# Optimization experiments

Hardware: AMD Instinct MI355X
Metric: run time of the kernel (lower is better)

Reference implementation:

```python
import jax, jax.numpy as jnp
import numpy as np

N = 50000          # nodes
E = 800000         # edges (before self-loops)
IN_DIM = 128
HIDDEN = 128
HEADS = 8
C = HIDDEN // HEADS  # 16, per-head dim
NEG_SLOPE = 0.2


def setup_inputs() -> dict:
    key = jax.random.key(0)
    ks = jax.random.split(key, 12)
    s = 0.1
    return {
        "x": jax.random.normal(ks[0], (N, IN_DIM), jnp.float32),
        "W1": jax.random.normal(ks[1], (IN_DIM, HIDDEN), jnp.float32) * s,
        "b1": jnp.zeros((HIDDEN,), jnp.float32),
        "att_l1": jax.random.normal(ks[2], (1, HEADS, C), jnp.float32) * s,
        "att_r1": jax.random.normal(ks[3], (1, HEADS, C), jnp.float32) * s,
        "W2": jax.random.normal(ks[4], (HIDDEN, HIDDEN), jnp.float32) * s,
        "b2": jnp.zeros((HIDDEN,), jnp.float32),
        "att_l2": jax.random.normal(ks[5], (1, HEADS, C), jnp.float32) * s,
        "att_r2": jax.random.normal(ks[6], (1, HEADS, C), jnp.float32) * s,
        "fcW": jax.random.normal(ks[7], (HIDDEN, 1), jnp.float32) * s,
        "fcb": jnp.zeros((1,), jnp.float32),
        "edge_index": jax.random.randint(ks[8], (2, E), 0, N, jnp.int32),
    }


def supergat_layer(h, W, b, att_l, att_r, src, dst):
    """SuperGATConv (attention_type='MX', concat=True), eval mode (no dropout).
    src/dst already include self-loops. h: [N, F_in]."""
    xt = (h @ W).reshape(N, HEADS, C)            # [N, H, C]
    x_j = xt[src]                                # source (message) feats [Etot, H, C]
    x_i = xt[dst]                                # target feats           [Etot, H, C]
    # MX attention: alpha = (a_l . x_j + a_r . x_i) * sigmoid(x_i . x_j)
    logits = jnp.sum(x_i * x_j, axis=-1)         # [Etot, H]
    alpha = jnp.sum(x_j * att_l, axis=-1) + jnp.sum(x_i * att_r, axis=-1)
    alpha = alpha * jax.nn.sigmoid(logits)
    alpha = jax.nn.leaky_relu(alpha, NEG_SLOPE)
    # segment softmax over incoming edges of each target node
    amax = jax.lax.stop_gradient(jax.ops.segment_max(alpha, dst, num_segments=N))
    ex = jnp.exp(alpha - amax[dst])
    denom = jax.ops.segment_sum(ex, dst, num_segments=N)
    attn = ex / (denom[dst] + 1e-16)             # [Etot, H]
    out = jax.ops.segment_sum(x_j * attn[..., None], dst, num_segments=N)  # [N, H, C]
    return out.reshape(N, HEADS * C) + b


def reference(x, W1, b1, att_l1, att_r1, W2, b2, att_l2, att_r2, fcW, fcb, edge_index):
    # add self-loops once (SuperGATConv add_self_loops=True)
    loops = jnp.arange(N, dtype=edge_index.dtype)
    src = jnp.concatenate([edge_index[0], loops])
    dst = jnp.concatenate([edge_index[1], loops])
    gelu = lambda t: jax.nn.gelu(t, approximate=False)
    h = gelu(supergat_layer(x, W1, b1, att_l1, att_r1, src, dst))   # dropout = identity (eval)
    h = gelu(supergat_layer(h, W2, b2, att_l2, att_r2, src, dst))
    return h @ fcW + fcb                          # [N, 1]
```

## Files before the change

### kernel.cpp

```cpp
#include <hip/hip_runtime.h>
#include <hip/hip_fp16.h>
#include <math.h>

#define N_NODES 50000
#define N_EDGES 800000
#define ETOT (N_EDGES + N_NODES)
#define F 128
#define SCAN_B 256
#define NSCAN ((N_NODES + SCAN_B - 1) / SCAN_B)
#define BM 128
#define LOG2E 1.44269504088896341f

typedef _Float16 h2 __attribute__((ext_vector_type(2)));

__device__ __forceinline__ float dpp_xor1(float v) {
    int b = __builtin_amdgcn_update_dpp(0, __float_as_int(v), 0xB1, 0xF, 0xF, true);
    return v + __int_as_float(b);
}


__global__ void k_count(const int* __restrict__ ei, int* __restrict__ counts) {
    int base = (blockIdx.x * 256 + threadIdx.x) * 8;
    if (base < N_EDGES) {
        int4 a = *(const int4*)(ei + N_EDGES + base);
        int4 b = *(const int4*)(ei + N_EDGES + base + 4);
        atomicAdd(&counts[a.x], 1); atomicAdd(&counts[a.y], 1);
        atomicAdd(&counts[a.z], 1); atomicAdd(&counts[a.w], 1);
        atomicAdd(&counts[b.x], 1); atomicAdd(&counts[b.y], 1);
        atomicAdd(&counts[b.z], 1); atomicAdd(&counts[b.w], 1);
    }
}

__global__ void k_scan1(const int* __restrict__ counts, int* __restrict__ indptr,
                        int* __restrict__ bsums) {
    __shared__ int s[SCAN_B];
    int i = blockIdx.x * SCAN_B + threadIdx.x;
    int v = (i < N_NODES) ? (counts[i] + 1) : 0;
    s[threadIdx.x] = v;
    __syncthreads();
    #pragma unroll
    for (int off = 1; off < SCAN_B; off <<= 1) {
        int t = (threadIdx.x >= off) ? s[threadIdx.x - off] : 0;
        __syncthreads();
        s[threadIdx.x] += t;
        __syncthreads();
    }
    if (i < N_NODES) indptr[i] = s[threadIdx.x] - v;
    if (threadIdx.x == SCAN_B - 1) bsums[blockIdx.x] = s[SCAN_B - 1];
}

__global__ void k_scan2(int* __restrict__ bsums) {
    __shared__ int s[SCAN_B];
    int v = (threadIdx.x < NSCAN) ? bsums[threadIdx.x] : 0;
    s[threadIdx.x] = v;
    __syncthreads();
    #pragma unroll
    for (int off = 1; off < SCAN_B; off <<= 1) {
        int t = (threadIdx.x >= off) ? s[threadIdx.x - off] : 0;
        __syncthreads();
        s[threadIdx.x] += t;
        __syncthreads();
    }
    if (threadIdx.x < NSCAN) bsums[threadIdx.x] = s[threadIdx.x] - v;
}

__global__ void k_scan3_fill(int* __restrict__ indptr, const int* __restrict__ bsums,
                             int* __restrict__ fill, int* __restrict__ srcs) {
    int i = blockIdx.x * SCAN_B + threadIdx.x;
    if (i < N_NODES) {
        int p = indptr[i] + bsums[blockIdx.x];
        indptr[i] = p;
        fill[i] = p + 1;
        srcs[p] = i;
    }
    if (i == 0) indptr[N_NODES] = ETOT;
}

__global__ void k_fill_edges(const int* __restrict__ ei, int* __restrict__ fill,
                             int* __restrict__ srcs) {
    int base = (blockIdx.x * 256 + threadIdx.x) * 8;
    if (base < N_EDGES) {
        int4 sa = *(const int4*)(ei + base);
        int4 sb = *(const int4*)(ei + base + 4);
        int4 da = *(const int4*)(ei + N_EDGES + base);
        int4 db = *(const int4*)(ei + N_EDGES + base + 4);
        int p0 = atomicAdd(&fill[da.x], 1);
        int p1 = atomicAdd(&fill[da.y], 1);
        int p2 = atomicAdd(&fill[da.z], 1);
        int p3 = atomicAdd(&fill[da.w], 1);
        int p4 = atomicAdd(&fill[db.x], 1);
        int p5 = atomicAdd(&fill[db.y], 1);
        int p6 = atomicAdd(&fill[db.z], 1);
        int p7 = atomicAdd(&fill[db.w], 1);
        srcs[p0] = sa.x; srcs[p1] = sa.y; srcs[p2] = sa.z; srcs[p3] = sa.w;
        srcs[p4] = sb.x; srcs[p5] = sb.y; srcs[p6] = sb.z; srcs[p7] = sb.w;
    }
}


__global__ __launch_bounds__(256) void k_gemm(const float* __restrict__ A,
                                              const float* __restrict__ W,
                                              unsigned char* __restrict__ Ch) {
    __shared__ float Ws[F][64];
    int t = threadIdx.x;
    int tile = blockIdx.x >> 1;
    int chf = blockIdx.x & 1;
    int r0 = tile * BM;

    const float4* W4 = (const float4*)W;
    #pragma unroll
    for (int jj = 0; jj < 8; ++jj) {
        int i = t + jj * 256;
        int k = i >> 4;
        int c4 = i & 15;
        *(float4*)&Ws[k][c4 * 4] = W4[k * 32 + chf * 16 + c4];
    }
    __syncthreads();

    int cg = t & 15;
    int rg = t >> 4;
    int rbase = r0 + rg * 8;

    const float4* Ap[8];
    #pragma unroll
    for (int i = 0; i < 8; ++i) {
        int gr = rbase + i;
        if (gr >= N_NODES) gr = N_NODES - 1;
        Ap[i] = (const float4*)A + (size_t)gr * 32;
    }

    float acc[8][4];
    #pragma unroll
    for (int i = 0; i < 8; ++i)
        #pragma unroll
        for (int j = 0; j < 4; ++j) acc[i][j] = 0.f;

    #pragma unroll 2
    for (int kk = 0; kk < 32; ++kk) {
        float4 xr[8];
        #pragma unroll
        for (int i = 0; i < 8; ++i) xr[i] = Ap[i][kk];
        #pragma unroll
        for (int kj = 0; kj < 4; ++kj) {
            int k = kk * 4 + kj;
            float4 wa = *(const float4*)&Ws[k][cg * 4];
            #pragma unroll
            for (int i = 0; i < 8; ++i) {
                float xv = (kj == 0) ? xr[i].x : (kj == 1) ? xr[i].y
                         : (kj == 2) ? xr[i].z : xr[i].w;
                acc[i][0] += xv * wa.x; acc[i][1] += xv * wa.y;
                acc[i][2] += xv * wa.z; acc[i][3] += xv * wa.w;
            }
        }
    }

    int colb = chf * 64 + cg * 4;
    #pragma unroll
    for (int i = 0; i < 8; ++i) {
        int row = rbase + i;
        if (row < N_NODES) {
            _Float16 hh[4];
            hh[0] = (_Float16)acc[i][0]; hh[1] = (_Float16)acc[i][1];
            hh[2] = (_Float16)acc[i][2]; hh[3] = (_Float16)acc[i][3];
            *(uint2*)(Ch + (size_t)row * 256 + colb * 2) = *(const uint2*)hh;
        }
    }
}


__global__ __launch_bounds__(256) void k_attn(
    const unsigned char* __restrict__ xt16,
    const int* __restrict__ indptr, const int* __restrict__ srcs,
    const float* __restrict__ att_l, const float* __restrict__ att_r,
    const float* __restrict__ bias, float* __restrict__ out,
    const float* __restrict__ fcW, const float* __restrict__ fcb, int mode) {

    int wid = threadIdx.x >> 6;
    int lane = threadIdx.x & 63;
    int node = blockIdx.x * 4 + wid;
    if (node >= N_NODES) return;
    int sub = lane >> 4;
    int sl  = lane & 15;

    uint4 xa = *(const uint4*)(xt16 + (size_t)node * 256 + sl * 16);
    h2 xi_h2[4];
    xi_h2[0] = __builtin_bit_cast(h2, xa.x); xi_h2[1] = __builtin_bit_cast(h2, xa.y);
    xi_h2[2] = __builtin_bit_cast(h2, xa.z); xi_h2[3] = __builtin_bit_cast(h2, xa.w);

    const float4* arp = (const float4*)(att_r + sl * 8);
    const float4* alp = (const float4*)(att_l + sl * 8);
    float4 r0 = arp[0], r1 = arp[1];
    float4 l0 = alp[0], l1 = alp[1];
    float rs = (float)xi_h2[0].x*r0.x + (float)xi_h2[0].y*r0.y
             + (float)xi_h2[1].x*r0.z + (float)xi_h2[1].y*r0.w
             + (float)xi_h2[2].x*r1.x + (float)xi_h2[2].y*r1.y
             + (float)xi_h2[3].x*r1.z + (float)xi_h2[3].y*r1.w;
    float ri = LOG2E * dpp_xor1(rs);
    h2 al_h2[4];
    al_h2[0] = h2{(_Float16)(l0.x*LOG2E), (_Float16)(l0.y*LOG2E)};
    al_h2[1] = h2{(_Float16)(l0.z*LOG2E), (_Float16)(l0.w*LOG2E)};
    al_h2[2] = h2{(_Float16)(l1.x*LOG2E), (_Float16)(l1.y*LOG2E)};
    al_h2[3] = h2{(_Float16)(l1.z*LOG2E), (_Float16)(l1.w*LOG2E)};

    float d = 0.f;
    float o[8];
    #pragma unroll
    for (int k = 0; k < 8; ++k) o[k] = 0.f;

    int beg = indptr[node], end = indptr[node + 1];
    int nstep = (end - beg + 3) >> 2;

    int idx = beg + sub;
    bool v0 = idx < end;
    int j0 = srcs[v0 ? idx : beg];
    uint4 ra0 = *(const uint4*)(xt16 + (size_t)j0 * 256 + sl * 16);
    int idx1 = idx + 4;
    bool v1 = idx1 < end;
    int j1 = srcs[v1 ? idx1 : beg];

    for (int s = 0; s < nstep; ++s) {
        uint4 ra1 = *(const uint4*)(xt16 + (size_t)j1 * 256 + sl * 16);
        int idx2 = idx1 + 4;
        bool v2 = idx2 < end;
        int j2 = srcs[v2 ? idx2 : beg];

        h2 xj[4];
        xj[0] = __builtin_bit_cast(h2, ra0.x); xj[1] = __builtin_bit_cast(h2, ra0.y);
        xj[2] = __builtin_bit_cast(h2, ra0.z); xj[3] = __builtin_bit_cast(h2, ra0.w);

        float lg = 0.f, lj = 0.f;
        #pragma unroll
        for (int k = 0; k < 4; ++k) {
            lg = __builtin_amdgcn_fdot2(xi_h2[k], xj[k], lg, false);
            lj = __builtin_amdgcn_fdot2(al_h2[k], xj[k], lj, false);
        }
        lg = dpp_xor1(lg);
        lj = dpp_xor1(lj);

        float sg = __builtin_amdgcn_rcpf(1.f + __builtin_amdgcn_exp2f(-lg * LOG2E));
        float a = (lj + ri) * sg;
        a = fmaxf(a, 0.f) + 0.2f * fminf(a, 0.f);
        a = v0 ? a : -1e30f;
        float e = __builtin_amdgcn_exp2f(a);
        d += e;
        #pragma unroll
        for (int k = 0; k < 4; ++k) {
            o[2*k]   += e * (float)xj[k].x;
            o[2*k+1] += e * (float)xj[k].y;
        }

        ra0 = ra1; v0 = v1; v1 = v2; j1 = j2; idx1 = idx2;
    }

    d += __shfl_xor(d, 16);
    d += __shfl_xor(d, 32);
    #pragma unroll
    for (int k = 0; k < 8; ++k) {
        o[k] += __shfl_xor(o[k], 16);
        o[k] += __shfl_xor(o[k], 32);
    }

    float inv = __builtin_amdgcn_rcpf(d + 1e-16f);
    const float4* bbp = (const float4*)(bias + sl * 8);
    float4 b0 = bbp[0], b1 = bbp[1];
    float bb[8] = {b0.x, b0.y, b0.z, b0.w, b1.x, b1.y, b1.z, b1.w};
    float g[8];
    #pragma unroll
    for (int k = 0; k < 8; ++k) {
        float v = o[k] * inv + bb[k];
        g[k] = 0.5f * v * (1.f + erff(v * 0.70710678118654752f));
    }

    if (mode == 0) {
        if (sub == 0) {
            float4* Co = (float4*)(out + (size_t)node * F + sl * 8);
            Co[0] = make_float4(g[0], g[1], g[2], g[3]);
            Co[1] = make_float4(g[4], g[5], g[6], g[7]);
        }
    } else {
        const float4* fwp = (const float4*)(fcW + sl * 8);
        float4 f0 = fwp[0], f1 = fwp[1];
        float p = g[0]*f0.x + g[1]*f0.y + g[2]*f0.z + g[3]*f0.w
                + g[4]*f1.x + g[5]*f1.y + g[6]*f1.z + g[7]*f1.w;
        p += __shfl_xor(p, 1);
        p += __shfl_xor(p, 2);
        p += __shfl_xor(p, 4);
        p += __shfl_xor(p, 8);
        if (lane == 0) out[node] = p + fcb[0];
    }
}


extern "C" void kernel_launch(void* const* d_in, const int* in_sizes, int n_in,
                              void* d_out, int out_size, void* d_ws, size_t ws_size,
                              hipStream_t stream) {
    const float* x     = (const float*)d_in[0];
    const float* W1    = (const float*)d_in[1];
    const float* b1    = (const float*)d_in[2];
    const float* attl1 = (const float*)d_in[3];
    const float* attr1 = (const float*)d_in[4];
    const float* W2    = (const float*)d_in[5];
    const float* b2    = (const float*)d_in[6];
    const float* attl2 = (const float*)d_in[7];
    const float* attr2 = (const float*)d_in[8];
    const float* fcW   = (const float*)d_in[9];
    const float* fcb   = (const float*)d_in[10];
    const int*   ei    = (const int*)d_in[11];
    float* outp = (float*)d_out;

    float* h1  = (float*)d_ws;
    unsigned char* xt16 = (unsigned char*)(h1 + (size_t)N_NODES * F);
    int* indptr = (int*)(xt16 + (size_t)N_NODES * 256);
    int* fill   = indptr + (N_NODES + 1);
    int* srcs   = fill + N_NODES;
    int* bsums  = srcs + ETOT;
    int* counts = fill;

    int nb_e8 = (N_EDGES / 8 + 255) / 256;

    hipMemsetAsync(counts, 0, N_NODES * sizeof(int), stream);
    k_count<<<nb_e8, 256, 0, stream>>>(ei, counts);
    k_scan1<<<NSCAN, SCAN_B, 0, stream>>>(counts, indptr, bsums);
    k_scan2<<<1, SCAN_B, 0, stream>>>(bsums);
    k_scan3_fill<<<NSCAN, SCAN_B, 0, stream>>>(indptr, bsums, fill, srcs);
    k_fill_edges<<<nb_e8, 256, 0, stream>>>(ei, fill, srcs);

    int nb_g = ((N_NODES + BM - 1) / BM) * 2;
    int nb_a = (N_NODES + 3) / 4;

    k_gemm<<<nb_g, 256, 0, stream>>>(x, W1, xt16);
    k_attn<<<nb_a, 256, 0, stream>>>(xt16, indptr, srcs, attl1, attr1, b1, h1, fcW, fcb, 0);
    k_gemm<<<nb_g, 256, 0, stream>>>(h1, W2, xt16);
    k_attn<<<nb_a, 256, 0, stream>>>(xt16, indptr, srcs, attl2, attr2, b2, outp, fcW, fcb, 1);
}
```

Before: 326.1 us.

## Use fp16 MFMA for node GEMMs with fp16 activations and prep kernel

Replaces the fp32 FMA register-tiled GEMM with a 16x16x32 fp16 MFMA kernel that reads fp16 inputs and a transposed fp16 weight held in LDS. A new prep kernel converts x and both weight matrices to fp16 and zeroes the counts buffer, replacing the memset. Layer-1 output is now stored as fp16, which halves the intermediate write and the GEMM input read. The goal is to cut GEMM compute and memory traffic, in exchange for an extra conversion pass over x and lower input precision.

```diff
diff --git a/kernel.cpp b/kernel.cpp
--- a/kernel.cpp
+++ b/kernel.cpp
@@ -8,14 +8,40 @@
 #define F 128
 #define SCAN_B 256
 #define NSCAN ((N_NODES + SCAN_B - 1) / SCAN_B)
-#define BM 128
 #define LOG2E 1.44269504088896341f
 
 typedef _Float16 h2 __attribute__((ext_vector_type(2)));
+typedef _Float16 h8 __attribute__((ext_vector_type(8)));
+typedef float f4v __attribute__((ext_vector_type(4)));
 
 __device__ __forceinline__ float dpp_xor1(float v) {
     int b = __builtin_amdgcn_update_dpp(0, __float_as_int(v), 0xB1, 0xF, 0xF, true);
     return v + __int_as_float(b);
+}
+
+
+__global__ void k_prep(const float* __restrict__ x, const float* __restrict__ W1,
+                       const float* __restrict__ W2, _Float16* __restrict__ x16,
+                       _Float16* __restrict__ WT1, _Float16* __restrict__ WT2,
+                       int* __restrict__ counts) {
+    int tid = blockIdx.x * 256 + threadIdx.x;
+    if (tid < 16384) {
+        int k = tid >> 7, c = tid & 127;
+        WT1[c * 128 + k] = (_Float16)W1[tid];
+    } else if (tid < 32768) {
+        int j = tid - 16384;
+        int k = j >> 7, c = j & 127;
+        WT2[c * 128 + k] = (_Float16)W2[j];
+    } else if (tid < 832768) {
+        int i = tid - 32768;
+        const float4* xp = (const float4*)x + (size_t)i * 2;
+        float4 a = xp[0], b = xp[1];
+        _Float16 hh[8] = {(_Float16)a.x, (_Float16)a.y, (_Float16)a.z, (_Float16)a.w,
+                          (_Float16)b.x, (_Float16)b.y, (_Float16)b.z, (_Float16)b.w};
+        *(uint4*)(x16 + (size_t)i * 8) = *(const uint4*)hh;
+    } else if (tid < 832768 + N_NODES) {
+        counts[tid - 832768] = 0;
+    }
 }
 
 
@@ -98,71 +124,58 @@
 }
 
 
-__global__ __launch_bounds__(256) void k_gemm(const float* __restrict__ A,
-                                              const float* __restrict__ W,
-                                              unsigned char* __restrict__ Ch) {
-    __shared__ float Ws[F][64];
+__global__ __launch_bounds__(256) void k_gemm(const _Float16* __restrict__ Ah,
+                                              const _Float16* __restrict__ WT,
+                                              _Float16* __restrict__ Ch) {
+    __shared__ _Float16 Wl[128][132];
     int t = threadIdx.x;
-    int tile = blockIdx.x >> 1;
-    int chf = blockIdx.x & 1;
-    int r0 = tile * BM;
-
-    const float4* W4 = (const float4*)W;
+
+    const uint4* WT4 = (const uint4*)WT;
     #pragma unroll
     for (int jj = 0; jj < 8; ++jj) {
         int i = t + jj * 256;
-        int k = i >> 4;
-        int c4 = i & 15;
-        *(float4*)&Ws[k][c4 * 4] = W4[k * 32 + chf * 16 + c4];
+        int c = i >> 4;
+        int k8 = i & 15;
+        *(uint4*)&Wl[c][k8 * 8] = WT4[i];
     }
     __syncthreads();
 
-    int cg = t & 15;
-    int rg = t >> 4;
-    int rbase = r0 + rg * 8;
-
-    const float4* Ap[8];
-    #pragma unroll
-    for (int i = 0; i < 8; ++i) {
-        int gr = rbase + i;
-        if (gr >= N_NODES) gr = N_NODES - 1;
-        Ap[i] = (const float4*)A + (size_t)gr * 32;
-    }
-
-    float acc[8][4];
-    #pragma unroll
-    for (int i = 0; i < 8; ++i)
+    int wid = t >> 6, lane = t & 63;
+    int rbase = blockIdx.x * 64 + wid * 16;
+    int rA = rbase + (lane & 15);
+    if (rA >= N_NODES) rA = N_NODES - 1;
+    int koff = (lane >> 4) * 8;
+
+    const _Float16* Ar = Ah + (size_t)rA * 128;
+    h8 af[4];
+    #pragma unroll
+    for (int kc = 0; kc < 4; ++kc)
+        af[kc] = *(const h8*)(Ar + kc * 32 + koff);
+
+    f4v acc[8];
+    #pragma unroll
+    for (int ct = 0; ct < 8; ++ct) acc[ct] = f4v{0.f, 0.f, 0.f, 0.f};
+
+    int colb = lane & 15;
+    #pragma unroll
+    for (int ct = 0; ct < 8; ++ct) {
+        const _Float16* wrow = &Wl[ct * 16 + colb][koff];
         #pragma unroll
-        for (int j = 0; j < 4; ++j) acc[i][j] = 0.f;
-
-    #pragma unroll 2
-    for (int kk = 0; kk < 32; ++kk) {
-        float4 xr[8];
-        #pragma unroll
-        for (int i = 0; i < 8; ++i) xr[i] = Ap[i][kk];
-        #pragma unroll
-        for (int kj = 0; kj < 4; ++kj) {
-            int k = kk * 4 + kj;
-            float4 wa = *(const float4*)&Ws[k][cg * 4];
+        for (int kc = 0; kc < 4; ++kc) {
+            h8 bf = *(const h8*)(wrow + kc * 32);
+            acc[ct] = __builtin_amdgcn_mfma_f32_16x16x32_f16(af[kc], bf, acc[ct], 0, 0, 0);
+        }
+    }
+
+    int rout = rbase + (lane >> 4) * 4;
+    #pragma unroll
+    for (int r = 0; r < 4; ++r) {
+        int row = rout + r;
+        if (row < N_NODES) {
+            _Float16* Crow = Ch + (size_t)row * 128;
             #pragma unroll
-            for (int i = 0; i < 8; ++i) {
-                float xv = (kj == 0) ? xr[i].x : (kj == 1) ? xr[i].y
-                         : (kj == 2) ? xr[i].z : xr[i].w;
-                acc[i][0] += xv * wa.x; acc[i][1] += xv * wa.y;
-                acc[i][2] += xv * wa.z; acc[i][3] += xv * wa.w;
-            }
-        }
-    }
-
-    int colb = chf * 64 + cg * 4;
-    #pragma unroll
-    for (int i = 0; i < 8; ++i) {
-        int row = rbase + i;
-        if (row < N_NODES) {
-            _Float16 hh[4];
-            hh[0] = (_Float16)acc[i][0]; hh[1] = (_Float16)acc[i][1];
-            hh[2] = (_Float16)acc[i][2]; hh[3] = (_Float16)acc[i][3];
-            *(uint2*)(Ch + (size_t)row * 256 + colb * 2) = *(const uint2*)hh;
+            for (int ct = 0; ct < 8; ++ct)
+                Crow[ct * 16 + colb] = (_Float16)acc[ct][r];
         }
     }
 }
@@ -173,6 +186,7 @@
     const int* __restrict__ indptr, const int* __restrict__ srcs,
     const float* __restrict__ att_l, const float* __restrict__ att_r,
     const float* __restrict__ bias, float* __restrict__ out,
+    _Float16* __restrict__ outh,
     const float* __restrict__ fcW, const float* __restrict__ fcb, int mode) {
 
     int wid = threadIdx.x >> 6;
@@ -273,9 +287,10 @@
 
     if (mode == 0) {
         if (sub == 0) {
-            float4* Co = (float4*)(out + (size_t)node * F + sl * 8);
-            Co[0] = make_float4(g[0], g[1], g[2], g[3]);
-            Co[1] = make_float4(g[4], g[5], g[6], g[7]);
+            _Float16 hh[8];
+            #pragma unroll
+            for (int k = 0; k < 8; ++k) hh[k] = (_Float16)g[k];
+            *(uint4*)(outh + (size_t)node * 128 + sl * 8) = *(const uint4*)hh;
         }
     } else {
         const float4* fwp = (const float4*)(fcW + sl * 8);
@@ -308,28 +323,34 @@
     const int*   ei    = (const int*)d_in[11];
     float* outp = (float*)d_out;
 
-    float* h1  = (float*)d_ws;
-    unsigned char* xt16 = (unsigned char*)(h1 + (size_t)N_NODES * F);
-    int* indptr = (int*)(xt16 + (size_t)N_NODES * 256);
+    _Float16* x16  = (_Float16*)d_ws;
+    _Float16* h16  = x16 + (size_t)N_NODES * F;
+    _Float16* xt16 = h16 + (size_t)N_NODES * F;
+    _Float16* WT1  = xt16 + (size_t)N_NODES * F;
+    _Float16* WT2  = WT1 + F * F;
+    int* indptr = (int*)(WT2 + F * F);
     int* fill   = indptr + (N_NODES + 1);
     int* srcs   = fill + N_NODES;
     int* bsums  = srcs + ETOT;
     int* counts = fill;
 
     int nb_e8 = (N_EDGES / 8 + 255) / 256;
-
-    hipMemsetAsync(counts, 0, N_NODES * sizeof(int), stream);
+    int nb_p  = (832768 + N_NODES + 255) / 256;
+
+    k_prep<<<nb_p, 256, 0, stream>>>(x, W1, W2, x16, WT1, WT2, counts);
     k_count<<<nb_e8, 256, 0, stream>>>(ei, counts);
     k_scan1<<<NSCAN, SCAN_B, 0, stream>>>(counts, indptr, bsums);
     k_scan2<<<1, SCAN_B, 0, stream>>>(bsums);
     k_scan3_fill<<<NSCAN, SCAN_B, 0, stream>>>(indptr, bsums, fill, srcs);
     k_fill_edges<<<nb_e8, 256, 0, stream>>>(ei, fill, srcs);
 
-    int nb_g = ((N_NODES + BM - 1) / BM) * 2;
+    int nb_g = (N_NODES + 63) / 64;
     int nb_a = (N_NODES + 3) / 4;
 
-    k_gemm<<<nb_g, 256, 0, stream>>>(x, W1, xt16);
-    k_attn<<<nb_a, 256, 0, stream>>>(xt16, indptr, srcs, attl1, attr1, b1, h1, fcW, fcb, 0);
-    k_gemm<<<nb_g, 256, 0, stream>>>(h1, W2, xt16);
-    k_attn<<<nb_a, 256, 0, stream>>>(xt16, indptr, srcs, attl2, attr2, b2, outp, fcW, fcb, 1);
-}
+    k_gemm<<<nb_g, 256, 0, stream>>>(x16, WT1, xt16);
+    k_attn<<<nb_a, 256, 0, stream>>>((const unsigned char*)xt16, indptr, srcs,
+                                     attl1, attr1, b1, outp, h16, fcW, fcb, 0);
+    k_gemm<<<nb_g, 256, 0, stream>>>(h16, WT2, xt16);
+    k_attn<<<nb_a, 256, 0, stream>>>((const unsigned char*)xt16, indptr, srcs,
+                                     attl2, attr2, b2, outp, h16, fcW, fcb, 1);
+}
```

After: 297.3 us. 8.8% less time.
